# Optimization experiments

Measured on AMD Instinct MI355X. Metric: run time of the kernel, lower is better.

The kernel has to match this reference:

```python
import jax, jax.numpy as jnp
import numpy as np

N_NODES = 20000


def gcn_layer(x, W, b, src, dst, n):
    # linear transform first (as in PyG GCNConv)
    h = x @ W  # [N, out]
    # add self-loops
    loop = jnp.arange(n, dtype=src.dtype)
    src_f = jnp.concatenate([src, loop])
    dst_f = jnp.concatenate([dst, loop])
    # symmetric degree normalization: deg computed on destination (col) index
    ones = jnp.ones_like(dst_f, dtype=h.dtype)
    deg = jax.ops.segment_sum(ones, dst_f, num_segments=n)
    dinv = jnp.where(deg > 0, jax.lax.rsqrt(deg), 0.0)
    norm = dinv[src_f] * dinv[dst_f]  # [E+N]
    # gather-normalize-scatter aggregation
    msgs = h[src_f] * norm[:, None]  # [E+N, out]
    out = jax.ops.segment_sum(msgs, dst_f, num_segments=n)
    return out + b


def setup_inputs() -> dict:
    key = jax.random.key(0)
    k = jax.random.split(key, 6)
    x = jax.random.normal(k[0], (N_NODES, 256), dtype=jnp.float32)
    edge_index = jax.random.randint(k[1], (2, 320000), 0, N_NODES, dtype=jnp.int64)
    s1 = 1.0 / np.sqrt(256)
    s2 = 1.0 / np.sqrt(1600)
    W1 = jax.random.uniform(k[2], (256, 1600), jnp.float32, -s1, s1)
    b1 = jnp.zeros((1600,), jnp.float32)
    W2 = jax.random.uniform(k[3], (1600, 400), jnp.float32, -s2, s2)
    b2 = jnp.zeros((400,), jnp.float32)
    return {"x": x, "edge_index": edge_index, "W1": W1, "b1": b1, "W2": W2, "b2": b2}


def reference(x, edge_index, W1, b1, W2, b2):
    src, dst = edge_index[0], edge_index[1]
    n = x.shape[0]
    h = jax.nn.relu(gcn_layer(x, W1, b1, src, dst, n))
    return gcn_layer(h, W2, b2, src, dst, n)
```

## Files before the change

### kernel.cpp

```cpp
#include <hip/hip_runtime.h>
#include <hip/hip_bf16.h>
#include <stdint.h>

typedef _Float16 f16;
typedef _Float16 f16x8 __attribute__((ext_vector_type(8)));
typedef _Float16 f16v4 __attribute__((ext_vector_type(4)));
typedef float f32x4 __attribute__((ext_vector_type(4)));

__device__ __forceinline__ void gload_lds16(const f16* g, f16* l) {
  __builtin_amdgcn_global_load_lds(
      (const __attribute__((address_space(1))) void*)g,
      (__attribute__((address_space(3))) void*)l, 16, 0, 0);
}

__device__ __forceinline__ int edge_at(const void* ep, int isI64, long long idx) {
  if (isI64) return (int)((const long long*)ep)[idx];
  return ((const int*)ep)[idx];
}

__global__ void detect_kernel(const unsigned int* __restrict__ e, int* __restrict__ flag) {
  __shared__ int any;
  if (threadIdx.x == 0) any = 0;
  __syncthreads();
  for (int idx = 1 + 2 * (int)threadIdx.x; idx < 4096; idx += 512) {
    if (e[idx] != 0u) any = 1;
  }
  __syncthreads();
  if (threadIdx.x == 0) flag[0] = any ? 0 : 1;
}

__global__ void deg_kernel(const void* __restrict__ ep, const int* __restrict__ flag,
                           int* __restrict__ indeg, int E) {
  int e = blockIdx.x * blockDim.x + threadIdx.x;
  if (e >= E) return;
  int i64 = flag[0];
  int d = edge_at(ep, i64, (long long)E + e);
  atomicAdd(&indeg[d], 1);
}

__global__ __launch_bounds__(1024) void prefix_kernel(const int* __restrict__ indeg,
                                                      int* __restrict__ rowptr,
                                                      float* __restrict__ dinv, int n) {
  __shared__ int wsum[16];
  int t = threadIdx.x;
  int lane = t & 63;
  int w = t >> 6;
  int carry = 0;
  if (t == 0) rowptr[0] = 0;
  for (int base = 0; base < n; base += 1024) {
    int i = base + t;
    int v = (i < n) ? indeg[i] : 0;
    if (i < n) dinv[i] = rsqrtf((float)(v + 1));
    int sv = v;
#pragma unroll
    for (int off = 1; off < 64; off <<= 1) {
      int u = __shfl_up(sv, off, 64);
      if (lane >= off) sv += u;
    }
    if (lane == 63) wsum[w] = sv;
    __syncthreads();
    if (w == 0 && lane < 16) {
      int ws = wsum[lane];
#pragma unroll
      for (int off = 1; off < 16; off <<= 1) {
        int u = __shfl_up(ws, off, 64);
        if (lane >= off) ws += u;
      }
      wsum[lane] = ws;
    }
    __syncthreads();
    int woff = (w > 0) ? wsum[w - 1] : 0;
    if (i < n) rowptr[i + 1] = carry + woff + sv;
    carry += wsum[15];
    __syncthreads();
  }
}

__global__ void scatter_kernel(const void* __restrict__ ep, const int* __restrict__ flag,
                               const int* __restrict__ rowptr, int* __restrict__ cursor,
                               int* __restrict__ colsrc, int E) {
  int e = blockIdx.x * blockDim.x + threadIdx.x;
  if (e >= E) return;
  int i64 = flag[0];
  int s = edge_at(ep, i64, (long long)e);
  int d = edge_at(ep, i64, (long long)E + e);
  int pos = atomicAdd(&cursor[d], 1);
  colsrc[rowptr[d] + pos] = s;
}

__global__ void xcast_kernel(const float* __restrict__ x, const float* __restrict__ dinv,
                             f16* __restrict__ xs, int n) {
  int c = blockIdx.x * 256 + threadIdx.x;
  if (c >= n * 64) return;
  int row = c >> 6;
  float d = dinv[row];
  float4 v = ((const float4*)x)[c];
  f16v4 r;
  r[0] = (f16)(d * v.x);
  r[1] = (f16)(d * v.y);
  r[2] = (f16)(d * v.z);
  r[3] = (f16)(d * v.w);
  ((f16v4*)xs)[c] = r;
}

__global__ __launch_bounds__(256) void agg1_kernel(const f16* __restrict__ xs,
                                                   const float* __restrict__ dinv,
                                                   const int* __restrict__ rowptr,
                                                   const int* __restrict__ colsrc,
                                                   f16* __restrict__ xa, int n) {
  int wave = threadIdx.x >> 6;
  int lane = threadIdx.x & 63;
  int i = blockIdx.x * 4 + wave;
  if (i >= n) return;
  const f16v4* xp = (const f16v4*)xs;
  float di = dinv[i];
  f16v4 s = xp[(size_t)i * 64 + lane];
  float a0 = (float)s[0], a1 = (float)s[1], a2 = (float)s[2], a3 = (float)s[3];
  float b0 = 0.f, b1 = 0.f, b2 = 0.f, b3 = 0.f;
  int beg = rowptr[i], end = rowptr[i + 1];
  int j = beg;
  for (; j + 3 < end; j += 4) {
    int s0 = colsrc[j], s1 = colsrc[j + 1], s2 = colsrc[j + 2], s3 = colsrc[j + 3];
    f16v4 v0 = xp[(size_t)s0 * 64 + lane];
    f16v4 v1 = xp[(size_t)s1 * 64 + lane];
    f16v4 v2 = xp[(size_t)s2 * 64 + lane];
    f16v4 v3 = xp[(size_t)s3 * 64 + lane];
    a0 += (float)v0[0] + (float)v2[0]; a1 += (float)v0[1] + (float)v2[1];
    a2 += (float)v0[2] + (float)v2[2]; a3 += (float)v0[3] + (float)v2[3];
    b0 += (float)v1[0] + (float)v3[0]; b1 += (float)v1[1] + (float)v3[1];
    b2 += (float)v1[2] + (float)v3[2]; b3 += (float)v1[3] + (float)v3[3];
  }
  for (; j < end; ++j) {
    int s0 = colsrc[j];
    f16v4 v0 = xp[(size_t)s0 * 64 + lane];
    a0 += (float)v0[0]; a1 += (float)v0[1]; a2 += (float)v0[2]; a3 += (float)v0[3];
  }
  f16v4 r;
  r[0] = (f16)(di * (a0 + b0));
  r[1] = (f16)(di * (a1 + b1));
  r[2] = (f16)(di * (a2 + b2));
  r[3] = (f16)(di * (a3 + b3));
  *(f16v4*)&xa[(size_t)i * 256 + lane * 4] = r;
}

__global__ __launch_bounds__(256) void agg2_kernel(const f16* __restrict__ gs,
                                                   const float* __restrict__ dinv,
                                                   const int* __restrict__ rowptr,
                                                   const int* __restrict__ colsrc,
                                                   const float* __restrict__ bias,
                                                   float* __restrict__ out, int n, int F) {
  int wave = threadIdx.x >> 6;
  int lane = threadIdx.x & 63;
  int i = blockIdx.x * 4 + wave;
  if (i >= n) return;
  int base = lane * 8;
  if (base >= F) return;
  float di = dinv[i];
  f16x8 sv = *(const f16x8*)&gs[(size_t)i * F + base];
  float a[8], b[8];
#pragma unroll
  for (int r = 0; r < 8; ++r) { a[r] = (float)sv[r]; b[r] = 0.f; }
  int beg = rowptr[i], end = rowptr[i + 1];
  int j = beg;
  for (; j + 3 < end; j += 4) {
    int s0 = colsrc[j], s1 = colsrc[j + 1], s2 = colsrc[j + 2], s3 = colsrc[j + 3];
    f16x8 v0 = *(const f16x8*)&gs[(size_t)s0 * F + base];
    f16x8 v1 = *(const f16x8*)&gs[(size_t)s1 * F + base];
    f16x8 v2 = *(const f16x8*)&gs[(size_t)s2 * F + base];
    f16x8 v3 = *(const f16x8*)&gs[(size_t)s3 * F + base];
#pragma unroll
    for (int r = 0; r < 8; ++r) {
      a[r] += (float)v0[r] + (float)v2[r];
      b[r] += (float)v1[r] + (float)v3[r];
    }
  }
  for (; j < end; ++j) {
    int s0 = colsrc[j];
    f16x8 v0 = *(const f16x8*)&gs[(size_t)s0 * F + base];
#pragma unroll
    for (int r = 0; r < 8; ++r) a[r] += (float)v0[r];
  }
  float4 o0, o1;
  float4 bv0 = *(const float4*)&bias[base];
  float4 bv1 = *(const float4*)&bias[base + 4];
  o0.x = di * (a[0] + b[0]) + bv0.x; o0.y = di * (a[1] + b[1]) + bv0.y;
  o0.z = di * (a[2] + b[2]) + bv0.z; o0.w = di * (a[3] + b[3]) + bv0.w;
  o1.x = di * (a[4] + b[4]) + bv1.x; o1.y = di * (a[5] + b[5]) + bv1.y;
  o1.z = di * (a[6] + b[6]) + bv1.z; o1.w = di * (a[7] + b[7]) + bv1.w;
  *(float4*)&out[(size_t)i * F + base] = o0;
  *(float4*)&out[(size_t)i * F + base + 4] = o1;
}

__global__ void castT_kernel(const float* __restrict__ W1, f16* __restrict__ W1t, int K1, int N1,
                             const float* __restrict__ W2, f16* __restrict__ W2t, int K2, int N2) {
  int idx = blockIdx.x * 256 + threadIdx.x;
  int t1 = K1 * N1;
  if (idx < t1) {
    int k = idx / N1;
    int nn = idx - k * N1;
    W1t[(size_t)nn * K1 + k] = (f16)W1[idx];
  } else {
    idx -= t1;
    if (idx < K2 * N2) {
      int k = idx / N2;
      int nn = idx - k * N2;
      W2t[(size_t)nn * K2 + k] = (f16)W2[idx];
    }
  }
}

__global__ __launch_bounds__(256) void gemm1_f16(
    const f16* __restrict__ A, const f16* __restrict__ B,
    const float* __restrict__ bias, f16* __restrict__ C,
    int M, int N, int K) {
  __shared__ __align__(16) f16 smem[2 * 128 * 64];
  f16* sA = smem;
  f16* sB = smem + 128 * 64;
  const int m0 = blockIdx.y * 128;
  const int n0 = blockIdx.x * 128;
  const int lane = threadIdx.x & 63;
  const int wave = threadIdx.x >> 6;
  const int wm = (wave & 1) * 64;
  const int wn = (wave >> 1) * 64;
  const int lrow = lane & 15;
  const int quad = lane >> 4;

  f32x4 acc[4][4];
#pragma unroll
  for (int i = 0; i < 4; ++i)
#pragma unroll
    for (int j = 0; j < 4; ++j) acc[i][j] = (f32x4)(0.f);

  for (int k0 = 0; k0 < K; k0 += 64) {
#pragma unroll
    for (int i = 0; i < 4; ++i) {
      int ch = (i * 4 + wave) * 64 + lane;
      int r = ch >> 3;
      int cg = (ch & 7) ^ (r & 7);
      int gr = min(m0 + r, M - 1);
      gload_lds16(&A[(size_t)gr * K + k0 + cg * 8], &sA[(size_t)(i * 4 + wave) * 512]);
      int gn = min(n0 + r, N - 1);
      gload_lds16(&B[(size_t)gn * K + k0 + cg * 8], &sB[(size_t)(i * 4 + wave) * 512]);
    }
    __syncthreads();
#pragma unroll
    for (int kk = 0; kk < 2; ++kk) {
      f16x8 af[4], bf[4];
      int cg = quad + kk * 4;
#pragma unroll
      for (int i = 0; i < 4; ++i) {
        int ra = wm + i * 16 + lrow;
        af[i] = *(const f16x8*)&sA[ra * 64 + ((cg ^ (ra & 7)) * 8)];
        int rb = wn + i * 16 + lrow;
        bf[i] = *(const f16x8*)&sB[rb * 64 + ((cg ^ (rb & 7)) * 8)];
      }
#pragma unroll
      for (int i = 0; i < 4; ++i)
#pragma unroll
        for (int j = 0; j < 4; ++j)
          acc[i][j] = __builtin_amdgcn_mfma_f32_16x16x32_f16(af[i], bf[j], acc[i][j], 0, 0, 0);
    }
    __syncthreads();
  }

  const int crow = quad * 4;
  const int ccol = lane & 15;
#pragma unroll
  for (int j = 0; j < 4; ++j) {
    int col = wn + j * 16 + ccol;
    int gcol = n0 + col;
    float bv = (gcol < N) ? bias[gcol] : 0.f;
#pragma unroll
    for (int i = 0; i < 4; ++i) {
#pragma unroll
      for (int r = 0; r < 4; ++r) {
        int row = wm + i * 16 + crow + r;
        smem[row * 128 + col] = (f16)fmaxf(acc[i][j][r] + bv, 0.f);
      }
    }
  }
  __syncthreads();
#pragma unroll
  for (int i = 0; i < 8; ++i) {
    int ch = i * 256 + (int)threadIdx.x;
    int r = ch >> 4;
    int cc = ch & 15;
    int grow = m0 + r;
    int gcol = n0 + cc * 8;
    if (grow < M && gcol < N)
      *(uint4*)&C[(size_t)grow * N + gcol] = *(const uint4*)&smem[r * 128 + cc * 8];
  }
}

__global__ __launch_bounds__(256) void gemm2_f16(
    const f16* __restrict__ A, const f16* __restrict__ B,
    const float* __restrict__ dinv, f16* __restrict__ C,
    int M, int N, int K) {
  __shared__ __align__(16) f16 smem[128 * 64 + 80 * 64];
  f16* sA = smem;
  f16* sB = smem + 128 * 64;

  const int mtc = (M + 127) >> 7;
  const int ntc = (N + 79) / 80;
  const int fullm = mtc & ~7;
  const int full = fullm * ntc;
  int idf = blockIdx.x;
  int mt, nt;
  if (idf < full) {
    int gsz = 8 * ntc;
    int grp = idf / gsz;
    int r = idf - grp * gsz;
    mt = grp * 8 + (r & 7);
    nt = r >> 3;
  } else {
    int r = idf - full;
    int rem = mtc - fullm;
    mt = fullm + r % rem;
    nt = r / rem;
  }
  const int m0 = mt * 128;
  const int n0 = nt * 80;
  const int lane = threadIdx.x & 63;
  const int wave = threadIdx.x >> 6;
  const int wm = wave * 32;
  const int lrow = lane & 15;
  const int quad = lane >> 4;

  f32x4 acc[2][5];
#pragma unroll
  for (int i = 0; i < 2; ++i)
#pragma unroll
    for (int j = 0; j < 5; ++j) acc[i][j] = (f32x4)(0.f);

  for (int k0 = 0; k0 < K; k0 += 64) {
#pragma unroll
    for (int i = 0; i < 4; ++i) {
      int ch = (i * 4 + wave) * 64 + lane;
      int r = ch >> 3;
      int cg = (ch & 7) ^ (r & 7);
      int gr = min(m0 + r, M - 1);
      gload_lds16(&A[(size_t)gr * K + k0 + cg * 8], &sA[(size_t)(i * 4 + wave) * 512]);
    }
#pragma unroll
    for (int i = 0; i < 3; ++i) {
      if (i * 4 + wave < 10) {
        int ch = (i * 4 + wave) * 64 + lane;
        int r = ch >> 3;
        int cg = (ch & 7) ^ (r & 7);
        gload_lds16(&B[(size_t)(n0 + r) * K + k0 + cg * 8], &sB[(size_t)(i * 4 + wave) * 512]);
      }
    }
    __syncthreads();
#pragma unroll
    for (int kk = 0; kk < 2; ++kk) {
      f16x8 af[2], bf[5];
      int cg = quad + kk * 4;
#pragma unroll
      for (int i = 0; i < 2; ++i) {
        int ra = wm + i * 16 + lrow;
        af[i] = *(const f16x8*)&sA[ra * 64 + ((cg ^ (ra & 7)) * 8)];
      }
#pragma unroll
      for (int j = 0; j < 5; ++j) {
        int rb = j * 16 + lrow;
        bf[j] = *(const f16x8*)&sB[rb * 64 + ((cg ^ (rb & 7)) * 8)];
      }
#pragma unroll
      for (int i = 0; i < 2; ++i)
#pragma unroll
        for (int j = 0; j < 5; ++j)
          acc[i][j] = __builtin_amdgcn_mfma_f32_16x16x32_f16(af[i], bf[j], acc[i][j], 0, 0, 0);
    }
    __syncthreads();
  }

  const int crow = quad * 4;
  const int ccol = lane & 15;
  float dsc[2][4];
#pragma unroll
  for (int i = 0; i < 2; ++i)
#pragma unroll
    for (int r = 0; r < 4; ++r) {
      int grow = m0 + wm + i * 16 + crow + r;
      dsc[i][r] = dinv[min(grow, M - 1)];
    }
#pragma unroll
  for (int j = 0; j < 5; ++j) {
    int col = j * 16 + ccol;
#pragma unroll
    for (int i = 0; i < 2; ++i) {
#pragma unroll
      for (int r = 0; r < 4; ++r) {
        int row = wm + i * 16 + crow + r;
        smem[row * 80 + col] = (f16)(acc[i][j][r] * dsc[i][r]);
      }
    }
  }
  __syncthreads();
#pragma unroll
  for (int i = 0; i < 5; ++i) {
    int ch = i * 256 + (int)threadIdx.x;
    int r = ch / 10;
    int rem = ch - 10 * r;
    int grow = m0 + r;
    if (grow < M)
      *(uint4*)&C[(size_t)grow * N + n0 + rem * 8] = *(const uint4*)&smem[r * 80 + rem * 8];
  }
}

extern "C" void kernel_launch(void* const* d_in, const int* in_sizes, int n_in,
                              void* d_out, int out_size, void* d_ws, size_t ws_size,
                              hipStream_t stream) {
  const float* x = (const float*)d_in[0];
  const void* edges = d_in[1];
  const float* W1 = (const float*)d_in[2];
  const float* b1 = (const float*)d_in[3];
  const float* W2 = (const float*)d_in[4];
  const float* b2 = (const float*)d_in[5];
  float* out = (float*)d_out;

  const int N1 = in_sizes[3];
  const int N2 = in_sizes[5];
  const int K1 = in_sizes[2] / N1;
  const int K2 = in_sizes[4] / N2;
  const int n = in_sizes[0] / K1;
  const int E = in_sizes[1] / 2;

  char* ws = (char*)d_ws;
  size_t o = 0;
  auto take = [&](size_t bytes) {
    char* p = ws + o;
    o += (bytes + 255) & ~(size_t)255;
    return p;
  };
  int* indeg = (int*)take((size_t)n * 4);
  int* cursor = (int*)take((size_t)n * 4);
  int* flag = (int*)take(4);
  size_t zero_bytes = o;
  int* rowptr = (int*)take((size_t)(n + 1) * 4);
  int* colsrc = (int*)take((size_t)E * 4);
  float* dinv = (float*)take((size_t)n * 4);
  f16* xs = (f16*)take((size_t)n * K1 * 2);
  f16* xa = (f16*)take((size_t)n * K1 * 2);
  f16* w1t = (f16*)take((size_t)K1 * N1 * 2);
  f16* w2t = (f16*)take((size_t)K2 * N2 * 2);
  f16* h = (f16*)take((size_t)n * N1 * 2);
  f16* g = (f16*)take((size_t)n * N2 * 2);

  hipMemsetAsync(d_ws, 0, zero_bytes, stream);

  detect_kernel<<<1, 256, 0, stream>>>((const unsigned int*)edges, flag);
  deg_kernel<<<(E + 255) / 256, 256, 0, stream>>>(edges, flag, indeg, E);
  prefix_kernel<<<1, 1024, 0, stream>>>(indeg, rowptr, dinv, n);
  scatter_kernel<<<(E + 255) / 256, 256, 0, stream>>>(edges, flag, rowptr, cursor, colsrc, E);

  castT_kernel<<<(K1 * N1 + K2 * N2 + 255) / 256, 256, 0, stream>>>(W1, w1t, K1, N1, W2, w2t,
                                                                    K2, N2);
  xcast_kernel<<<(n * 64 + 255) / 256, 256, 0, stream>>>(x, dinv, xs, n);

  agg1_kernel<<<(n + 3) / 4, 256, 0, stream>>>(xs, dinv, rowptr, colsrc, xa, n);
  {
    dim3 grid((N1 + 127) / 128, (n + 127) / 128);
    gemm1_f16<<<grid, 256, 0, stream>>>(xa, w1t, b1, h, n, N1, K1);
  }
  {
    int mtc = (n + 127) / 128;
    int ntc = (N2 + 79) / 80;
    gemm2_f16<<<mtc * ntc, 256, 0, stream>>>(h, w2t, dinv, g, n, N2, K2);
  }
  agg2_kernel<<<(n + 3) / 4, 256, 0, stream>>>(g, dinv, rowptr, colsrc, b2, out, n, N2);
}
```

Baseline: 291.9 us.

## Fuse preprocessing kernels, parallelize prefix scan, double-buffer gemm2 LDS tiles

Merges detect with the weight cast/transpose and scatter with the x cast into combined launches to cut kernel launch count. Replaces the single-block serial prefix scan with a two-kernel multi-block reduce-then-scan. Double-buffers gemm2's shared-memory tiles so the next K slice loads while MFMAs run, which doubles its LDS footprint and may reduce occupancy. It also clamps B row indices in gemm2. The block-sum scan assumes at most 64 blocks.

```diff
diff --git a/kernel.cpp b/kernel.cpp
--- a/kernel.cpp
+++ b/kernel.cpp
@@ -18,15 +18,36 @@
   return ((const int*)ep)[idx];
 }
 
-__global__ void detect_kernel(const unsigned int* __restrict__ e, int* __restrict__ flag) {
-  __shared__ int any;
-  if (threadIdx.x == 0) any = 0;
-  __syncthreads();
-  for (int idx = 1 + 2 * (int)threadIdx.x; idx < 4096; idx += 512) {
-    if (e[idx] != 0u) any = 1;
-  }
-  __syncthreads();
-  if (threadIdx.x == 0) flag[0] = any ? 0 : 1;
+__global__ void detect_castT_kernel(const unsigned int* __restrict__ e, int* __restrict__ flag,
+                                    const float* __restrict__ W1, f16* __restrict__ W1t,
+                                    int K1, int N1,
+                                    const float* __restrict__ W2, f16* __restrict__ W2t,
+                                    int K2, int N2) {
+  if (blockIdx.x == 0) {
+    __shared__ int any;
+    if (threadIdx.x == 0) any = 0;
+    __syncthreads();
+    for (int idx = 1 + 2 * (int)threadIdx.x; idx < 4096; idx += 512) {
+      if (e[idx] != 0u) any = 1;
+    }
+    __syncthreads();
+    if (threadIdx.x == 0) flag[0] = any ? 0 : 1;
+    return;
+  }
+  int idx = (blockIdx.x - 1) * 256 + threadIdx.x;
+  int t1 = K1 * N1;
+  if (idx < t1) {
+    int k = idx / N1;
+    int nn = idx - k * N1;
+    W1t[(size_t)nn * K1 + k] = (f16)W1[idx];
+  } else {
+    idx -= t1;
+    if (idx < K2 * N2) {
+      int k = idx / N2;
+      int nn = idx - k * N2;
+      W2t[(size_t)nn * K2 + k] = (f16)W2[idx];
+    }
+  }
 }
 
 __global__ void deg_kernel(const void* __restrict__ ep, const int* __restrict__ flag,
@@ -38,59 +59,87 @@
   atomicAdd(&indeg[d], 1);
 }
 
-__global__ __launch_bounds__(1024) void prefix_kernel(const int* __restrict__ indeg,
-                                                      int* __restrict__ rowptr,
-                                                      float* __restrict__ dinv, int n) {
+__global__ __launch_bounds__(1024) void scan1_kernel(const int* __restrict__ indeg,
+                                                     float* __restrict__ dinv,
+                                                     int* __restrict__ bsum, int n) {
+  __shared__ int ws[16];
+  int t = threadIdx.x;
+  int i = blockIdx.x * 1024 + t;
+  int v = (i < n) ? indeg[i] : 0;
+  if (i < n) dinv[i] = rsqrtf((float)(v + 1));
+  int s = v;
+#pragma unroll
+  for (int off = 32; off > 0; off >>= 1) s += __shfl_down(s, off, 64);
+  if ((t & 63) == 0) ws[t >> 6] = s;
+  __syncthreads();
+  if (t < 16) {
+    int x = ws[t];
+#pragma unroll
+    for (int off = 8; off > 0; off >>= 1) x += __shfl_down(x, off, 64);
+    if (t == 0) bsum[blockIdx.x] = x;
+  }
+}
+
+__global__ __launch_bounds__(1024) void scan3_kernel(const int* __restrict__ indeg,
+                                                     const int* __restrict__ bsum,
+                                                     int* __restrict__ rowptr, int n, int nb) {
   __shared__ int wsum[16];
+  __shared__ int bexcl[64];
   int t = threadIdx.x;
   int lane = t & 63;
   int w = t >> 6;
-  int carry = 0;
-  if (t == 0) rowptr[0] = 0;
-  for (int base = 0; base < n; base += 1024) {
-    int i = base + t;
-    int v = (i < n) ? indeg[i] : 0;
-    if (i < n) dinv[i] = rsqrtf((float)(v + 1));
-    int sv = v;
+  int i = blockIdx.x * 1024 + t;
+  int v = (i < n) ? indeg[i] : 0;
+  int sv = v;
+#pragma unroll
+  for (int off = 1; off < 64; off <<= 1) {
+    int u = __shfl_up(sv, off, 64);
+    if (lane >= off) sv += u;
+  }
+  if (lane == 63) wsum[w] = sv;
+  __syncthreads();
+  if (w == 0) {
+    if (lane < 16) {
+      int x = wsum[lane];
+#pragma unroll
+      for (int off = 1; off < 16; off <<= 1) {
+        int u = __shfl_up(x, off, 64);
+        if (lane >= off) x += u;
+      }
+      wsum[lane] = x;
+    }
+    int bv = (lane < nb) ? bsum[lane] : 0;
+    int bs = bv;
 #pragma unroll
     for (int off = 1; off < 64; off <<= 1) {
-      int u = __shfl_up(sv, off, 64);
-      if (lane >= off) sv += u;
-    }
-    if (lane == 63) wsum[w] = sv;
-    __syncthreads();
-    if (w == 0 && lane < 16) {
-      int ws = wsum[lane];
-#pragma unroll
-      for (int off = 1; off < 16; off <<= 1) {
-        int u = __shfl_up(ws, off, 64);
-        if (lane >= off) ws += u;
-      }
-      wsum[lane] = ws;
-    }
-    __syncthreads();
-    int woff = (w > 0) ? wsum[w - 1] : 0;
-    if (i < n) rowptr[i + 1] = carry + woff + sv;
-    carry += wsum[15];
-    __syncthreads();
-  }
-}
-
-__global__ void scatter_kernel(const void* __restrict__ ep, const int* __restrict__ flag,
-                               const int* __restrict__ rowptr, int* __restrict__ cursor,
-                               int* __restrict__ colsrc, int E) {
-  int e = blockIdx.x * blockDim.x + threadIdx.x;
-  if (e >= E) return;
-  int i64 = flag[0];
-  int s = edge_at(ep, i64, (long long)e);
-  int d = edge_at(ep, i64, (long long)E + e);
-  int pos = atomicAdd(&cursor[d], 1);
-  colsrc[rowptr[d] + pos] = s;
-}
-
-__global__ void xcast_kernel(const float* __restrict__ x, const float* __restrict__ dinv,
-                             f16* __restrict__ xs, int n) {
-  int c = blockIdx.x * 256 + threadIdx.x;
+      int u = __shfl_up(bs, off, 64);
+      if (lane >= off) bs += u;
+    }
+    bexcl[lane] = bs - bv;
+  }
+  __syncthreads();
+  int woff = (w > 0) ? wsum[w - 1] : 0;
+  if (i < n) rowptr[i + 1] = bexcl[blockIdx.x] + woff + sv;
+  if (i == 0) rowptr[0] = 0;
+}
+
+__global__ void scatter_xcast_kernel(const void* __restrict__ ep, const int* __restrict__ flag,
+                                     const int* __restrict__ rowptr, int* __restrict__ cursor,
+                                     int* __restrict__ colsrc, int E, int sb,
+                                     const float* __restrict__ x, const float* __restrict__ dinv,
+                                     f16* __restrict__ xs, int n) {
+  int b = blockIdx.x;
+  if (b < sb) {
+    int e = b * 256 + threadIdx.x;
+    if (e >= E) return;
+    int i64 = flag[0];
+    int s = edge_at(ep, i64, (long long)e);
+    int d = edge_at(ep, i64, (long long)E + e);
+    int pos = atomicAdd(&cursor[d], 1);
+    colsrc[rowptr[d] + pos] = s;
+    return;
+  }
+  int c = (b - sb) * 256 + threadIdx.x;
   if (c >= n * 64) return;
   int row = c >> 6;
   float d = dinv[row];
@@ -191,24 +240,6 @@
   *(float4*)&out[(size_t)i * F + base + 4] = o1;
 }
 
-__global__ void castT_kernel(const float* __restrict__ W1, f16* __restrict__ W1t, int K1, int N1,
-                             const float* __restrict__ W2, f16* __restrict__ W2t, int K2, int N2) {
-  int idx = blockIdx.x * 256 + threadIdx.x;
-  int t1 = K1 * N1;
-  if (idx < t1) {
-    int k = idx / N1;
-    int nn = idx - k * N1;
-    W1t[(size_t)nn * K1 + k] = (f16)W1[idx];
-  } else {
-    idx -= t1;
-    if (idx < K2 * N2) {
-      int k = idx / N2;
-      int nn = idx - k * N2;
-      W2t[(size_t)nn * K2 + k] = (f16)W2[idx];
-    }
-  }
-}
-
 __global__ __launch_bounds__(256) void gemm1_f16(
     const f16* __restrict__ A, const f16* __restrict__ B,
     const float* __restrict__ bias, f16* __restrict__ C,
@@ -292,13 +323,12 @@
   }
 }
 
+#define G2TILE (128 * 64 + 80 * 64)
 __global__ __launch_bounds__(256) void gemm2_f16(
     const f16* __restrict__ A, const f16* __restrict__ B,
     const float* __restrict__ dinv, f16* __restrict__ C,
     int M, int N, int K) {
-  __shared__ __align__(16) f16 smem[128 * 64 + 80 * 64];
-  f16* sA = smem;
-  f16* sB = smem + 128 * 64;
+  __shared__ __align__(16) f16 smem[2 * G2TILE];
 
   const int mtc = (M + 127) >> 7;
   const int ntc = (N + 79) / 80;
@@ -332,7 +362,9 @@
 #pragma unroll
     for (int j = 0; j < 5; ++j) acc[i][j] = (f32x4)(0.f);
 
-  for (int k0 = 0; k0 < K; k0 += 64) {
+  auto stage = [&](int k0, int buf) {
+    f16* sA = smem + buf * G2TILE;
+    f16* sB = sA + 128 * 64;
 #pragma unroll
     for (int i = 0; i < 4; ++i) {
       int ch = (i * 4 + wave) * 64 + lane;
@@ -347,10 +379,19 @@
         int ch = (i * 4 + wave) * 64 + lane;
         int r = ch >> 3;
         int cg = (ch & 7) ^ (r & 7);
-        gload_lds16(&B[(size_t)(n0 + r) * K + k0 + cg * 8], &sB[(size_t)(i * 4 + wave) * 512]);
-      }
-    }
+        int gn = min(n0 + r, N - 1);
+        gload_lds16(&B[(size_t)gn * K + k0 + cg * 8], &sB[(size_t)(i * 4 + wave) * 512]);
+      }
+    }
+  };
+
+  stage(0, 0);
+  int buf = 0;
+  for (int k0 = 0; k0 < K; k0 += 64) {
     __syncthreads();
+    if (k0 + 64 < K) stage(k0 + 64, buf ^ 1);
+    const f16* sA = smem + buf * G2TILE;
+    const f16* sB = sA + 128 * 64;
 #pragma unroll
     for (int kk = 0; kk < 2; ++kk) {
       f16x8 af[2], bf[5];
@@ -371,9 +412,10 @@
         for (int j = 0; j < 5; ++j)
           acc[i][j] = __builtin_amdgcn_mfma_f32_16x16x32_f16(af[i], bf[j], acc[i][j], 0, 0, 0);
     }
-    __syncthreads();
-  }
-
+    buf ^= 1;
+  }
+
+  __syncthreads();
   const int crow = quad * 4;
   const int ccol = lane & 15;
   float dsc[2][4];
@@ -440,6 +482,7 @@
   int* rowptr = (int*)take((size_t)(n + 1) * 4);
   int* colsrc = (int*)take((size_t)E * 4);
   float* dinv = (float*)take((size_t)n * 4);
+  int* bsum = (int*)take(64 * 4);
   f16* xs = (f16*)take((size_t)n * K1 * 2);
   f16* xa = (f16*)take((size_t)n * K1 * 2);
   f16* w1t = (f16*)take((size_t)K1 * N1 * 2);
@@ -449,14 +492,18 @@
 
   hipMemsetAsync(d_ws, 0, zero_bytes, stream);
 
-  detect_kernel<<<1, 256, 0, stream>>>((const unsigned int*)edges, flag);
-  deg_kernel<<<(E + 255) / 256, 256, 0, stream>>>(edges, flag, indeg, E);
-  prefix_kernel<<<1, 1024, 0, stream>>>(indeg, rowptr, dinv, n);
-  scatter_kernel<<<(E + 255) / 256, 256, 0, stream>>>(edges, flag, rowptr, cursor, colsrc, E);
-
-  castT_kernel<<<(K1 * N1 + K2 * N2 + 255) / 256, 256, 0, stream>>>(W1, w1t, K1, N1, W2, w2t,
-                                                                    K2, N2);
-  xcast_kernel<<<(n * 64 + 255) / 256, 256, 0, stream>>>(x, dinv, xs, n);
+  const int nb = (n + 1023) / 1024;
+  const int castBlocks = (K1 * N1 + K2 * N2 + 255) / 256;
+  const int sb = (E + 255) / 256;
+  const int xcastBlocks = (n * 64 + 255) / 256;
+
+  detect_castT_kernel<<<1 + castBlocks, 256, 0, stream>>>((const unsigned int*)edges, flag, W1,
+                                                          w1t, K1, N1, W2, w2t, K2, N2);
+  deg_kernel<<<sb, 256, 0, stream>>>(edges, flag, indeg, E);
+  scan1_kernel<<<nb, 1024, 0, stream>>>(indeg, dinv, bsum, n);
+  scan3_kernel<<<nb, 1024, 0, stream>>>(indeg, bsum, rowptr, n, nb);
+  scatter_xcast_kernel<<<sb + xcastBlocks, 256, 0, stream>>>(edges, flag, rowptr, cursor, colsrc,
+                                                             E, sb, x, dinv, xs, n);
 
   agg1_kernel<<<(n + 3) / 4, 256, 0, stream>>>(xs, dinv, rowptr, colsrc, xa, n);
   {
```

Result: faster. 264.9 us (-9.3%).
